# Performance work log

Measured on AMD Instinct MI355X. Metric: run time of the kernel, lower is better.

The kernel has to match this reference:

```python
import jax, jax.numpy as jnp
import numpy as np
import math

SAMPLE_RATIO = 0.25
K = 5
EPS = 1e-6

def _cells(loc_orig, H, W):
    # map normalized [-1,1] coords to nearest grid cell index, as in tcformer token2map/map2token
    loc = jnp.clip(loc_orig, -1.0, 1.0)
    px = jnp.clip(jnp.round(0.5 * (loc[..., 0] + 1.0) * W - 0.5).astype(jnp.int32), 0, W - 1)
    py = jnp.clip(jnp.round(0.5 * (loc[..., 1] + 1.0) * H - 0.5).astype(jnp.int32), 0, H - 1)
    return py * W + px  # [B, N0]

def token2map(x, loc_orig, idx_agg, H, W):
    B, N, C = x.shape
    N0 = loc_orig.shape[1]
    cell = _cells(loc_orig, H, W)
    seg = (cell + jnp.arange(B)[:, None] * (H * W)).reshape(-1)
    feat = x[jnp.arange(B)[:, None], idx_agg]  # [B, N0, C] token feature per original point
    sums = jax.ops.segment_sum(feat.reshape(-1, C), seg, num_segments=B * H * W)
    cnt = jax.ops.segment_sum(jnp.ones((B * N0,), x.dtype), seg, num_segments=B * H * W)
    x_map = sums / (cnt[:, None] + EPS)  # per-cell mean over points hitting the cell
    return x_map.reshape(B, H, W, C).transpose(0, 3, 1, 2)

def map2token(x_map, N, loc_orig, idx_agg, agg_weight):
    B, C, H, W = x_map.shape
    cell = _cells(loc_orig, H, W)
    val = x_map.reshape(B, C, H * W).transpose(0, 2, 1)  # [B, HW, C]
    vpt = val[jnp.arange(B)[:, None], cell]              # [B, N0, C] map value at each point
    seg = (idx_agg + jnp.arange(B)[:, None] * N).reshape(-1)
    w = agg_weight.reshape(-1)
    wsum = jax.ops.segment_sum(w, seg, num_segments=B * N) + EPS
    ssum = jax.ops.segment_sum(vpt.reshape(-1, C) * w[:, None], seg, num_segments=B * N)
    return (ssum / wsum[:, None]).reshape(B, N, C)  # agg_weight-weighted mean per token

def token_cluster_merge(x, Ns, idx_agg, weight, k):
    B, N, C = x.shape
    # DPC-KNN clustering (index computation; mirrors torch.no_grad block)
    sq = jnp.sum(x * x, -1)
    d2 = jnp.clip(sq[:, :, None] + sq[:, None, :] - 2.0 * jnp.einsum('bnc,bmc->bnm', x, x), 0.0, None)
    dist = jnp.sqrt(d2) / (C ** 0.5)
    dnear = -jax.lax.top_k(-dist, k)[0]                  # k smallest distances (incl. self)
    density = jnp.exp(-jnp.mean(dnear * dnear, -1))
    mask = density[:, None, :] > density[:, :, None]
    dmax = jnp.max(dist.reshape(B, -1), -1)[:, None, None]
    parent_dist = jnp.min(jnp.where(mask, dist, dmax), -1)  # dist to nearest higher-density token
    score = parent_dist * density
    index_down = jax.lax.top_k(score, Ns)[1]             # [B, Ns] cluster centers
    idx_cluster = jnp.argmin(dist[jnp.arange(B)[:, None], index_down], axis=1)  # [B, N]
    idx_cluster = idx_cluster.at[jnp.arange(B)[:, None], index_down].set(jnp.arange(Ns)[None, :])
    # weighted merge of tokens into clusters
    seg = (idx_cluster + jnp.arange(B)[:, None] * Ns).reshape(-1)
    w = weight.reshape(-1)
    allw = jax.ops.segment_sum(w, seg, num_segments=B * Ns) + EPS
    norm_w = (w / allw[seg]).reshape(B, N)
    x_merged = jax.ops.segment_sum((x * norm_w[:, :, None]).reshape(-1, C), seg, num_segments=B * Ns).reshape(B, Ns, C)
    idx_agg_down = idx_cluster[jnp.arange(B)[:, None], idx_agg]      # compose index maps
    weight_t = norm_w[jnp.arange(B)[:, None], idx_agg][..., None]    # [B, N0, 1]
    return x_merged, idx_agg_down, weight_t

def _forward(x, loc_orig, idx_agg, agg_weight, idx_k_loc, H, W, conv_w, conv_b, skip_w, ln_g, ln_b, conf_w, conf_b):
    B, N, C = x.shape
    x_map = token2map(x, loc_orig, idx_agg, H, W)
    x_map = jax.lax.conv_general_dilated(x_map, conv_w, (2, 2), ((1, 1), (1, 1))) + conv_b[None, :, None, None]
    x_tok = map2token(x_map, N, loc_orig, idx_agg, agg_weight) + jnp.einsum('bnc,oc->bno', x, skip_w)
    mu = jnp.mean(x_tok, -1, keepdims=True)
    var = jnp.mean((x_tok - mu) ** 2, -1, keepdims=True)
    x_tok = (x_tok - mu) / jnp.sqrt(var + 1e-5) * ln_g + ln_b
    conf = jnp.einsum('bnc,oc->bno', x_tok, conf_w) + conf_b
    weight = jnp.exp(conf)
    Ns = max(math.ceil(N * SAMPLE_RATIO), 1)
    x_down, idx_agg_down, weight_t = token_cluster_merge(x_tok, Ns, idx_agg, weight, K)
    agg_weight_down = agg_weight * weight_t
    agg_weight_down = agg_weight_down / jnp.max(agg_weight_down, axis=1, keepdims=True)
    # down_block is an injected submodule; treated as identity passthrough here
    return x_down, idx_agg_down, agg_weight_down

def setup_inputs():
    key = jax.random.key(0)
    ks = jax.random.split(key, 8)
    B, N, C, N0, Cout = 8, 256, 256, 16384, 512
    return {
        'x': jax.random.normal(ks[0], (B, N, C), jnp.float32),
        'loc_orig': jax.random.uniform(ks[1], (B, N0, 2), jnp.float32, -1.0, 1.0),
        'idx_agg': jax.random.randint(ks[2], (B, N0), 0, N),
        'agg_weight': jax.random.uniform(ks[3], (B, N0, 1), jnp.float32, 0.1, 1.0),
        'idx_k_loc': jax.random.randint(ks[4], (B, N0, K), 0, N0),
        'H': 64, 'W': 64,
        'conv_w': jax.random.normal(ks[5], (Cout, C, 3, 3), jnp.float32) * 0.02,
        'conv_b': jnp.zeros((Cout,), jnp.float32),
        'skip_w': jax.random.normal(ks[6], (Cout, C), jnp.float32) * 0.02,
        'ln_g': jnp.ones((Cout,), jnp.float32),
        'ln_b': jnp.zeros((Cout,), jnp.float32),
        'conf_w': jax.random.normal(ks[7], (1, Cout), jnp.float32) * 0.02,
        'conf_b': jnp.zeros((1,), jnp.float32),
    }

def reference(x, loc_orig, idx_agg, agg_weight, idx_k_loc, H, W, conv_w, conv_b, skip_w, ln_g, ln_b, conf_w, conf_b):
    return _forward(x, loc_orig, idx_agg, agg_weight, idx_k_loc, H, W, conv_w, conv_b, skip_w, ln_g, ln_b, conf_w, conf_b)
```

## Files before the change

kernel.cpp:

```cpp
#include <hip/hip_runtime.h>
#include <math.h>

typedef unsigned long long ull;
typedef __attribute__((ext_vector_type(8))) short short8v;
typedef __attribute__((ext_vector_type(4))) float float4v;

#define NB   8
#define NTOK 256
#define CIN  256
#define NP   16384
#define NCO  512
#define HW64 4096
#define OHW  1024
#define NS   64
#define EPS  1e-6f
#define KC   2304
#define NKC  72

constexpr size_t OFF_SUMS = 0;
constexpr size_t OFF_CNT  = OFF_SUMS + (size_t)NB*HW64*CIN;
constexpr size_t OFF_AMAT = OFF_CNT  + (size_t)NB*HW64;
constexpr size_t OFF_ALLW = OFF_AMAT + (size_t)NB*NTOK*OHW;
constexpr size_t OFF_DMAX = OFF_ALLW + (size_t)NB*NS;
constexpr size_t OFF_MAXW = OFF_DMAX + NB;
constexpr size_t ZERO_END = OFF_MAXW + NB;
constexpr size_t OFF_WT   = ZERO_END;
constexpr size_t OFF_SKWT = OFF_WT   + (size_t)KC*NCO;
constexpr size_t OFF_Y    = OFF_SKWT + (size_t)CIN*NCO;
constexpr size_t OFF_C2   = OFF_Y    + (size_t)NB*OHW*NCO;
constexpr size_t OFF_WSUM = OFF_C2   + (size_t)NB*NTOK*NCO;
constexpr size_t OFF_XSKIP= OFF_WSUM + (size_t)NB*NTOK;
constexpr size_t OFF_XTOK = OFF_XSKIP+ (size_t)NB*NTOK*NCO;
constexpr size_t OFF_XPK  = OFF_XTOK + (size_t)NB*NTOK*NCO;
constexpr size_t OFF_WEXP = OFF_XPK  + (size_t)NB*NTOK*NCO;
constexpr size_t OFF_SQ   = OFF_WEXP + (size_t)NB*NTOK;
constexpr size_t OFF_DIST = OFF_SQ   + (size_t)NB*NTOK;
constexpr size_t OFF_DENS = OFF_DIST + (size_t)NB*NTOK*NTOK;
constexpr size_t OFF_SCORE= OFF_DENS + (size_t)NB*NTOK;
constexpr size_t OFF_IND  = OFF_SCORE+ (size_t)NB*NTOK;
constexpr size_t OFF_IDXCL= OFF_IND  + (size_t)NB*NS;
constexpr size_t OFF_NORMW= OFF_IDXCL+ (size_t)NB*NTOK;
constexpr size_t OFF_AWBUF= OFF_NORMW+ (size_t)NB*NTOK;
constexpr size_t OFF_XTPK = OFF_AWBUF+ (size_t)NB*NP;
constexpr size_t OFF_XTOKPK= OFF_Y;

__device__ __forceinline__ unsigned pack_hl(float x) {
    unsigned u = __float_as_uint(x);
    unsigned t = u + 0x7fffu + ((u >> 16) & 1u);
    unsigned hibits = t & 0xffff0000u;
    float lo = x - __uint_as_float(hibits);
    unsigned ul = __float_as_uint(lo);
    unsigned lt = ul + 0x7fffu + ((ul >> 16) & 1u);
    return hibits | (lt >> 16);
}
__device__ __forceinline__ unsigned f2bf(float f) {
    unsigned u = __float_as_uint(f);
    return (u + 0x7fffu + ((u >> 16) & 1u)) >> 16;
}
__device__ __forceinline__ unsigned hp2(unsigned w0, unsigned w1) {
    return __builtin_amdgcn_perm(w1, w0, 0x07060302u);
}
__device__ __forceinline__ unsigned lp2(unsigned w0, unsigned w1) {
    return __builtin_amdgcn_perm(w1, w0, 0x05040100u);
}

__global__ void hist(const float* __restrict__ loc, const int* __restrict__ idxagg,
                     const float* __restrict__ aggw,
                     int* __restrict__ cntmat, float* __restrict__ cnt,
                     float* __restrict__ amat) {
    int bp = blockIdx.x*256 + threadIdx.x;
    int b  = bp >> 14;
    float lx = loc[2*bp+0], ly = loc[2*bp+1];
    lx = fminf(fmaxf(lx, -1.f), 1.f);
    ly = fminf(fmaxf(ly, -1.f), 1.f);
    int px = (int)rintf((lx + 1.f)*32.f - 0.5f); px = min(max(px,0),63);
    int py = (int)rintf((ly + 1.f)*32.f - 0.5f); py = min(max(py,0),63);
    int cell = py*64 + px;
    int tok = idxagg[bp];
    atomicAdd(&cntmat[((size_t)(b*HW64 + cell))*NTOK + tok], 1);
    atomicAdd(&cnt[b*HW64 + cell], 1.0f);
    int qx = (int)rintf((lx + 1.f)*16.f - 0.5f); qx = min(max(qx,0),31);
    int qy = (int)rintf((ly + 1.f)*16.f - 0.5f); qy = min(max(qy,0),31);
    atomicAdd(&amat[((size_t)(b*NTOK + tok))*OHW + qy*32 + qx], aggw[bp]);
}

__global__ void xpack_both(const float* __restrict__ x, unsigned* __restrict__ xtpk,
                           unsigned* __restrict__ xpk) {
    int id = blockIdx.x*256 + threadIdx.x;
    int tok = id & 255, cin = (id >> 8) & 255, b = id >> 16;
    unsigned pk = pack_hl(x[((size_t)(b*NTOK + tok))*CIN + cin]);
    xtpk[id] = pk;
    xpk[((size_t)(b*NTOK + tok))*CIN + cin] = pk;
}

__global__ void wtrans(const float* __restrict__ convw, uint4* __restrict__ wtf) {
    int tid = blockIdx.x*256 + threadIdx.x;
    int lane = tid & 63;
    int r1 = tid >> 6;
    int h = r1 & 1;
    int r2 = r1 >> 1;
    int f = r2 & 3;
    int r3 = r2 >> 2;
    int kc = r3 % NKC, mt = r3 / NKC;
    int cout = mt*64 + f*16 + (lane & 15);
    int kb = kc*32 + (lane >> 4)*8;
    unsigned s[8];
    #pragma unroll
    for (int j = 0; j < 8; ++j) {
        int k = kb + j;
        int grp = k >> 8, cin = k & 255;
        unsigned w = pack_hl(convw[(size_t)cout*KC + cin*9 + grp]);
        s[j] = h ? (w & 0xffffu) : (w >> 16);
    }
    uint4 o;
    o.x = s[0] | (s[1]<<16); o.y = s[2] | (s[3]<<16);
    o.z = s[4] | (s[5]<<16); o.w = s[6] | (s[7]<<16);
    wtf[tid] = o;
}

__global__ void pack4(const float4* __restrict__ src, uint4* __restrict__ dst) {
    size_t i = (size_t)blockIdx.x*256 + threadIdx.x;
    float4 v = src[i];
    uint4 o;
    o.x = pack_hl(v.x); o.y = pack_hl(v.y); o.z = pack_hl(v.z); o.w = pack_hl(v.w);
    dst[i] = o;
}

__launch_bounds__(512)
__global__ void map_gemm(const int* __restrict__ A, const unsigned* __restrict__ B,
                         const float* __restrict__ cnt, unsigned* __restrict__ xmapu) {
    __shared__ __align__(16) unsigned short Ah[4096];
    __shared__ __align__(16) unsigned short Bh[8192], Bl[8192];
    int z = blockIdx.z, m0 = blockIdx.y*128;
    const int* Ab = A + ((size_t)z*HW64 + m0)*NTOK;
    const unsigned* Bb = B + (size_t)z*CIN*NTOK;
    int t = threadIdx.x, lane = t & 63;
    int w = t >> 6;
    int wm = w >> 2, wn = w & 3;
    int l15 = lane & 15, l4 = lane >> 4;
    int rowA = t & 127, kgA = t >> 7;
    int rowB = t & 255, kgB0 = (t >> 8)*2;
    const int* arow = Ab + (size_t)rowA*NTOK + kgA*8;
    const unsigned* brow = Bb + (size_t)rowB*NTOK + kgB0*8;
    int wbA = (rowA>>4)*512 + kgA*128 + (rowA&15)*8;
    int wbB = (rowB>>4)*512 + kgB0*128 + (rowB&15)*8;

    float4v acc[4][4] = {};
    int4 ia0, ia1;
    uint4 rb[2][2];
    auto loadA = [&](int kc) {
        const int* p = arow + kc*32;
        ia0 = *(const int4*)p; ia1 = *(const int4*)(p + 4);
    };
    auto loadB = [&](int kc) {
        #pragma unroll
        for (int s = 0; s < 2; ++s) {
            const unsigned* p = brow + kc*32 + s*8;
            rb[s][0] = *(const uint4*)p; rb[s][1] = *(const uint4*)(p + 4);
        }
    };
    loadA(0); loadB(0);

    for (int kc = 0; kc < 8; ++kc) {
        __syncthreads();
        uint4 h, l;
        h.x = f2bf((float)ia0.x) | (f2bf((float)ia0.y) << 16);
        h.y = f2bf((float)ia0.z) | (f2bf((float)ia0.w) << 16);
        h.z = f2bf((float)ia1.x) | (f2bf((float)ia1.y) << 16);
        h.w = f2bf((float)ia1.z) | (f2bf((float)ia1.w) << 16);
        *(uint4*)&Ah[wbA] = h;
        #pragma unroll
        for (int s = 0; s < 2; ++s) {
            uint4 u0 = rb[s][0], u1 = rb[s][1];
            h.x=hp2(u0.x,u0.y); h.y=hp2(u0.z,u0.w); h.z=hp2(u1.x,u1.y); h.w=hp2(u1.z,u1.w);
            l.x=lp2(u0.x,u0.y); l.y=lp2(u0.z,u0.w); l.z=lp2(u1.x,u1.y); l.w=lp2(u1.z,u1.w);
            *(uint4*)&Bh[wbB + s*128] = h; *(uint4*)&Bl[wbB + s*128] = l;
        }
        __syncthreads();
        if (kc < 7) { loadA(kc+1); loadB(kc+1); }

        short8v bh[4], bl[4];
        #pragma unroll
        for (int q = 0; q < 4; ++q) {
            int off = (wn*4 + q)*512 + l4*128 + l15*8;
            bh[q] = *(const short8v*)&Bh[off];
            bl[q] = *(const short8v*)&Bl[off];
        }
        #pragma unroll
        for (int p = 0; p < 4; ++p) {
            int off = (wm*4 + p)*512 + l4*128 + l15*8;
            short8v ah = *(const short8v*)&Ah[off];
            #pragma unroll
            for (int q = 0; q < 4; ++q) {
                acc[p][q] = __builtin_amdgcn_mfma_f32_16x16x32_bf16(ah, bh[q], acc[p][q], 0, 0, 0);
                acc[p][q] = __builtin_amdgcn_mfma_f32_16x16x32_bf16(ah, bl[q], acc[p][q], 0, 0, 0);
            }
        }
    }

    const float* cntb = cnt + (size_t)z*HW64;
    #pragma unroll
    for (int p = 0; p < 4; ++p) {
        int mb = m0 + wm*64 + p*16 + l4*4;
        #pragma unroll
        for (int q = 0; q < 4; ++q) {
            int n = wn*64 + q*16 + l15;
            #pragma unroll
            for (int r = 0; r < 4; ++r) {
                float v = acc[p][q][r] / (cntb[mb + r] + EPS);
                xmapu[((size_t)z*HW64 + mb + r)*CIN + n] = pack_hl(v);
            }
        }
    }
}

__launch_bounds__(256)
__global__ void conv_gemm(const unsigned* __restrict__ xmap, const uint4* __restrict__ wtf,
                          const float* __restrict__ convb, unsigned* __restrict__ ytp) {
    __shared__ __align__(16) unsigned short Ahi[2][4096], Alo[2][4096];
    int bid = blockIdx.x;
    int mt = bid & 7;
    int xt = bid >> 3;
    int n0 = xt * 128;
    int m0 = mt * 64;
    int t = threadIdx.x;
    int lane = t & 63, wid = t >> 6;
    int wm = wid >> 1, wn = wid & 1;
    int l15 = lane & 15, l4 = lane >> 4;

    int rowL = t & 127, kg = t >> 7;
    int posG = n0 + rowL;
    int bb = posG >> 10, rem = posG & 1023;
    int oy = rem >> 5, ox = rem & 31;

    int wbA0 = (rowL>>4)*512 + kg*128 + (rowL&15)*8;
    int wbA1 = wbA0 + 256;

    float4v acc[4][2] = {};
    uint4 a00,a01,a10,a11;

    auto loadA = [&](int kc) {
        int grp = kc >> 3;
        int ky = grp/3, kx = grp - 3*ky;
        int iy = 2*oy - 1 + ky, ix = 2*ox - 1 + kx;
        if ((unsigned)iy < 64u && (unsigned)ix < 64u) {
            const unsigned* ap = xmap + ((((size_t)bb*64 + iy)*64 + ix)*256 + (kc&7)*32 + kg*8);
            a00 = *(const uint4*)ap;       a01 = *(const uint4*)(ap + 4);
            a10 = *(const uint4*)(ap + 16); a11 = *(const uint4*)(ap + 20);
        } else {
            a00 = make_uint4(0,0,0,0); a01 = a00; a10 = a00; a11 = a00;
        }
    };
    auto repackA = [&](int buf) {
        uint4 h, l;
        h.x=hp2(a00.x,a00.y); h.y=hp2(a00.z,a00.w); h.z=hp2(a01.x,a01.y); h.w=hp2(a01.z,a01.w);
        l.x=lp2(a00.x,a00.y); l.y=lp2(a00.z,a00.w); l.z=lp2(a01.x,a01.y); l.w=lp2(a01.z,a01.w);
        *(uint4*)&Ahi[buf][wbA0] = h; *(uint4*)&Alo[buf][wbA0] = l;
        h.x=hp2(a10.x,a10.y); h.y=hp2(a10.z,a10.w); h.z=hp2(a11.x,a11.y); h.w=hp2(a11.z,a11.w);
        l.x=lp2(a10.x,a10.y); l.y=lp2(a10.z,a10.w); l.z=lp2(a11.x,a11.y); l.w=lp2(a11.z,a11.w);
        *(uint4*)&Ahi[buf][wbA1] = h; *(uint4*)&Alo[buf][wbA1] = l;
    };
    const uint4* wbase = wtf + ((size_t)(((mt*NKC)*4 + wn*2)*2))*64 + lane;

    short8v bhc[2], blc[2], bhn[2], bln[2];
    #pragma unroll
    for (int q = 0; q < 2; ++q) {
        bhc[q] = *(const short8v*)(wbase + q*128);
        blc[q] = *(const short8v*)(wbase + q*128 + 64);
    }
    loadA(0);
    repackA(0);
    __syncthreads();
    int cur = 0;

    for (int kc = 0; kc < NKC; ++kc) {
        bool nl = (kc + 1 < NKC);
        if (nl) {
            loadA(kc+1);
            const uint4* wb = wbase + (size_t)(kc+1)*512;
            #pragma unroll
            for (int q = 0; q < 2; ++q) {
                bhn[q] = *(const short8v*)(wb + q*128);
                bln[q] = *(const short8v*)(wb + q*128 + 64);
            }
        }
        #pragma unroll
        for (int p = 0; p < 4; ++p) {
            int off = (wm*4 + p)*512 + l4*128 + l15*8;
            short8v ah = *(const short8v*)&Ahi[cur][off];
            short8v al = *(const short8v*)&Alo[cur][off];
            #pragma unroll
            for (int q = 0; q < 2; ++q) {
                acc[p][q] = __builtin_amdgcn_mfma_f32_16x16x32_bf16(ah, bhc[q], acc[p][q], 0, 0, 0);
                acc[p][q] = __builtin_amdgcn_mfma_f32_16x16x32_bf16(ah, blc[q], acc[p][q], 0, 0, 0);
                acc[p][q] = __builtin_amdgcn_mfma_f32_16x16x32_bf16(al, bhc[q], acc[p][q], 0, 0, 0);
            }
        }
        if (nl) {
            repackA(cur ^ 1);
            #pragma unroll
            for (int q = 0; q < 2; ++q) { bhc[q] = bhn[q]; blc[q] = bln[q]; }
        }
        __syncthreads();
        cur ^= 1;
    }

    int bbk = n0 >> 10;
    int pos0 = (n0 & 1023) + wm*64;
    #pragma unroll
    for (int p = 0; p < 4; ++p) {
        int posb = pos0 + p*16 + l4*4;
        #pragma unroll
        for (int q = 0; q < 2; ++q) {
            int col = m0 + wn*32 + q*16 + l15;
            float bv = convb[col];
            uint4 o;
            o.x = pack_hl(acc[p][q][0] + bv);
            o.y = pack_hl(acc[p][q][1] + bv);
            o.z = pack_hl(acc[p][q][2] + bv);
            o.w = pack_hl(acc[p][q][3] + bv);
            *(uint4*)&ytp[((size_t)(bbk*NCO + col))*OHW + posb] = o;
        }
    }
}

template<int MODE, int TM, int TN, int AF>
__launch_bounds__(256)
__global__ void gemm_pk(const void* __restrict__ Av, const unsigned* __restrict__ B,
                        float* __restrict__ C, int K, int N,
                        long sA, long sB, long sC,
                        const float* __restrict__ aux, unsigned* __restrict__ dmaxU) {
    constexpr int NA = TM/64, NBs = TN/64;
    constexpr int WSM = TM/64;
    constexpr int WSN = 4/WSM;
    constexpr int TWM = TM/WSM, TWN = TN/WSN;
    constexpr int P = TWM/16, Q = TWN/16;
    __shared__ __align__(16) unsigned short Ahi[TM*32], Alo[TM*32];
    __shared__ __align__(16) unsigned short Bhi[TN*32], Blo[TN*32];
    int z = blockIdx.z;
    const unsigned* Ab = (const unsigned*)Av + (size_t)z*sA;
    const unsigned* Bb = B + (size_t)z*sB;
    float* Cb = C + (size_t)z*sC;
    int n0 = blockIdx.x*TN, m0 = blockIdx.y*TM;
    int t = threadIdx.x;
    int lane = t & 63, wid = t >> 6;
    int wm = (WSM==2) ? (wid >> 1) : 0;
    int wn = (WSM==2) ? (wid & 1)  : wid;
    int l15 = lane & 15, l4 = lane >> 4;

    int rowA = t & (TM-1), kgA = t / TM;
    int rowB = t & (TN-1), kgB = t / TN;
    const unsigned* arow = Ab + (size_t)(m0 + rowA)*K + kgA*8;
    const unsigned* brw  = Bb + (size_t)(n0 + rowB)*K + kgB*8;
    int wbA = (rowA>>4)*512 + kgA*128 + (rowA&15)*8;
    int wbB = (rowB>>4)*512 + kgB*128 + (rowB&15)*8;

    float4v acc[P][Q] = {};
    uint4 ra[NA][2], rb[NBs][2];
    auto loadA = [&](int kc) {
        #pragma unroll
        for (int s = 0; s < NA; ++s) {
            const unsigned* p = arow + (size_t)kc*32 + s*16;
            ra[s][0] = *(const uint4*)p; ra[s][1] = *(const uint4*)(p + 4);
        }
    };
    auto loadB = [&](int kc) {
        #pragma unroll
        for (int s = 0; s < NBs; ++s) {
            const unsigned* p = brw + (size_t)kc*32 + s*16;
            rb[s][0] = *(const uint4*)p; rb[s][1] = *(const uint4*)(p + 4);
        }
    };
    loadA(0); loadB(0);
    int nkc = K >> 5;

    for (int kc = 0; kc < nkc; ++kc) {
        __syncthreads();
        uint4 h, l;
        #pragma unroll
        for (int s = 0; s < NA; ++s) {
            uint4 u0 = ra[s][0], u1 = ra[s][1];
            if (AF == 0) {
                h.x=hp2(u0.x,u0.y); h.y=hp2(u0.z,u0.w); h.z=hp2(u1.x,u1.y); h.w=hp2(u1.z,u1.w);
                l.x=lp2(u0.x,u0.y); l.y=lp2(u0.z,u0.w); l.z=lp2(u1.x,u1.y); l.w=lp2(u1.z,u1.w);
            } else {
                unsigned pk0 = pack_hl(__uint_as_float(u0.x)), pk1 = pack_hl(__uint_as_float(u0.y));
                unsigned pk2 = pack_hl(__uint_as_float(u0.z)), pk3 = pack_hl(__uint_as_float(u0.w));
                unsigned pk4 = pack_hl(__uint_as_float(u1.x)), pk5 = pack_hl(__uint_as_float(u1.y));
                unsigned pk6 = pack_hl(__uint_as_float(u1.z)), pk7 = pack_hl(__uint_as_float(u1.w));
                h.x = (pk0>>16) | (pk1 & 0xffff0000u); h.y = (pk2>>16) | (pk3 & 0xffff0000u);
                h.z = (pk4>>16) | (pk5 & 0xffff0000u); h.w = (pk6>>16) | (pk7 & 0xffff0000u);
                l.x = (pk0&0xffffu) | (pk1<<16); l.y = (pk2&0xffffu) | (pk3<<16);
                l.z = (pk4&0xffffu) | (pk5<<16); l.w = (pk6&0xffffu) | (pk7<<16);
            }
            *(uint4*)&Ahi[wbA + s*256] = h; *(uint4*)&Alo[wbA + s*256] = l;
        }
        #pragma unroll
        for (int s = 0; s < NBs; ++s) {
            uint4 u0 = rb[s][0], u1 = rb[s][1];
            h.x=hp2(u0.x,u0.y); h.y=hp2(u0.z,u0.w); h.z=hp2(u1.x,u1.y); h.w=hp2(u1.z,u1.w);
            l.x=lp2(u0.x,u0.y); l.y=lp2(u0.z,u0.w); l.z=lp2(u1.x,u1.y); l.w=lp2(u1.z,u1.w);
            *(uint4*)&Bhi[wbB + s*256] = h; *(uint4*)&Blo[wbB + s*256] = l;
        }
        __syncthreads();
        if (kc + 1 < nkc) { loadA(kc+1); loadB(kc+1); }

        short8v bh[Q], bl[Q];
        #pragma unroll
        for (int q = 0; q < Q; ++q) {
            int off = (wn*Q + q)*512 + l4*128 + l15*8;
            bh[q] = *(const short8v*)&Bhi[off];
            bl[q] = *(const short8v*)&Blo[off];
        }
        #pragma unroll
        for (int p = 0; p < P; ++p) {
            int off = (wm*P + p)*512 + l4*128 + l15*8;
            short8v ah = *(const short8v*)&Ahi[off];
            short8v al = *(const short8v*)&Alo[off];
            #pragma unroll
            for (int q = 0; q < Q; ++q) {
                acc[p][q] = __builtin_amdgcn_mfma_f32_16x16x32_bf16(ah, bh[q], acc[p][q], 0, 0, 0);
                acc[p][q] = __builtin_amdgcn_mfma_f32_16x16x32_bf16(ah, bl[q], acc[p][q], 0, 0, 0);
                acc[p][q] = __builtin_amdgcn_mfma_f32_16x16x32_bf16(al, bh[q], acc[p][q], 0, 0, 0);
            }
        }
    }

    if (MODE == 0) {
        #pragma unroll
        for (int p = 0; p < P; ++p) {
            int mb = m0 + wm*TWM + p*16 + l4*4;
            #pragma unroll
            for (int q = 0; q < Q; ++q) {
                int n = n0 + wn*TWN + q*16 + l15;
                #pragma unroll
                for (int r = 0; r < 4; ++r)
                    Cb[(size_t)(mb + r)*N + n] = acc[p][q][r];
            }
        }
    } else {
        const float inv = 1.0f / sqrtf(512.0f);
        const float* sqb = aux + (size_t)z*NTOK;
        float tmax = 0.f;
        #pragma unroll
        for (int p = 0; p < P; ++p) {
            int mb = m0 + wm*TWM + p*16 + l4*4;
            #pragma unroll
            for (int q = 0; q < Q; ++q) {
                int n = n0 + wn*TWN + q*16 + l15;
                float sn = sqb[n];
                #pragma unroll
                for (int r = 0; r < 4; ++r) {
                    float d2 = sqb[mb + r] + sn - 2.0f*acc[p][q][r];
                    float d = sqrtf(fmaxf(d2, 0.0f)) * inv;
                    Cb[(size_t)(mb + r)*N + n] = d;
                    tmax = fmaxf(tmax, d);
                }
            }
        }
        __shared__ float redm[4];
        #pragma unroll
        for (int off = 32; off; off >>= 1) tmax = fmaxf(tmax, __shfl_xor(tmax, off, 64));
        if (lane == 0) redm[wid] = tmax;
        __syncthreads();
        if (t == 0) {
            float m = fmaxf(fmaxf(redm[0], redm[1]), fmaxf(redm[2], redm[3]));
            atomicMax(dmaxU + z, __float_as_uint(m));
        }
    }
}

__global__ void wsum_rows(const float* __restrict__ amat, float* __restrict__ wsum) {
    int row = blockIdx.x*4 + (threadIdx.x >> 6);
    int lane = threadIdx.x & 63;
    const float* ar = amat + (size_t)row*OHW;
    float s = 0.f;
    #pragma unroll
    for (int r = 0; r < 16; ++r) s += ar[lane + 64*r];
    #pragma unroll
    for (int off = 32; off; off >>= 1) s += __shfl_xor(s, off, 64);
    if (lane == 0) wsum[row] = s;
}

__device__ __forceinline__ float block_sum256(float v, float* red) {
    #pragma unroll
    for (int off = 32; off; off >>= 1) v += __shfl_xor(v, off, 64);
    __syncthreads();
    if ((threadIdx.x & 63) == 0) red[threadIdx.x >> 6] = v;
    __syncthreads();
    return red[0] + red[1] + red[2] + red[3];
}

__global__ void ln_conf(const float* __restrict__ C2, const float* __restrict__ wsum,
                        const float* __restrict__ xskip, const float* __restrict__ g,
                        const float* __restrict__ be, const float* __restrict__ confw,
                        const float* __restrict__ confb, float* __restrict__ xtok,
                        unsigned* __restrict__ xtokpk,
                        float* __restrict__ wexp, float* __restrict__ sqv) {
    __shared__ float red[4];
    int row = blockIdx.x, t = threadIdx.x;
    float ws = wsum[row] + EPS;
    size_t base = (size_t)row*NCO;
    float v0 = C2[base + t]       / ws + xskip[base + t];
    float v1 = C2[base + t + 256] / ws + xskip[base + t + 256];
    float mu  = block_sum256(v0 + v1, red) / 512.0f;
    float d0 = v0 - mu, d1 = v1 - mu;
    float var = block_sum256(d0*d0 + d1*d1, red) / 512.0f;
    float sv = sqrtf(var + 1e-5f);
    float x0 = d0/sv * g[t]       + be[t];
    float x1 = d1/sv * g[t + 256] + be[t + 256];
    xtok[base + t] = x0;
    xtok[base + t + 256] = x1;
    xtokpk[base + t] = pack_hl(x0);
    xtokpk[base + t + 256] = pack_hl(x1);
    float cs = block_sum256(x0*confw[t] + x1*confw[t + 256], red);
    float qs = block_sum256(x0*x0 + x1*x1, red);
    if (t == 0) {
        wexp[row] = expf(cs + confb[0]);
        sqv[row]  = qs;
    }
}

__global__ void knn_dens(const float* __restrict__ dist, float* __restrict__ dens) {
    int row = blockIdx.x*4 + (threadIdx.x >> 6);
    int lane = threadIdx.x & 63;
    const float* dr = dist + (size_t)row*NTOK;
    float v0 = dr[lane], v1 = dr[lane+64], v2 = dr[lane+128], v3 = dr[lane+192];
    float acc = 0.f;
    #pragma unroll
    for (int it = 0; it < 5; ++it) {
        float lm = fminf(fminf(v0, v1), fminf(v2, v3));
        float gm = lm;
        #pragma unroll
        for (int off = 32; off; off >>= 1) gm = fminf(gm, __shfl_xor(gm, off, 64));
        acc += gm*gm;
        ull ball = __ballot(lm == gm);
        int first = __ffsll(ball) - 1;
        if (lane == first) {
            if      (v0 == gm) v0 = 1e30f;
            else if (v1 == gm) v1 = 1e30f;
            else if (v2 == gm) v2 = 1e30f;
            else               v3 = 1e30f;
        }
    }
    if (lane == 0) dens[row] = expf(-(acc/5.0f));
}

__global__ void parent_score(const float* __restrict__ dist, const float* __restrict__ dens,
                             const unsigned* __restrict__ dmaxU, float* __restrict__ score) {
    int row = blockIdx.x*4 + (threadIdx.x >> 6);
    int lane = threadIdx.x & 63;
    int b = row >> 8;
    float di = dens[row];
    float dm = __uint_as_float(dmaxU[b]);
    const float* dr = dist + (size_t)row*NTOK;
    const float* db = dens + (size_t)b*NTOK;
    float pd = dm;
    #pragma unroll
    for (int r = 0; r < 4; ++r) {
        int j = lane + 64*r;
        pd = fminf(pd, (db[j] > di) ? dr[j] : dm);
    }
    #pragma unroll
    for (int off = 32; off; off >>= 1) pd = fminf(pd, __shfl_xor(pd, off, 64));
    if (lane == 0) score[row] = pd * di;
}

__global__ void topk64(const float* __restrict__ score, int* __restrict__ ind) {
    int b = blockIdx.x, lane = threadIdx.x;
    const float* sb = score + b*NTOK;
    ull k0, k1, k2, k3;
    {
        unsigned i0 = lane, i1 = lane+64, i2 = lane+128, i3 = lane+192;
        k0 = ((ull)(__float_as_uint(sb[i0]) + 1u) << 32) | (unsigned)(4095 - i0);
        k1 = ((ull)(__float_as_uint(sb[i1]) + 1u) << 32) | (unsigned)(4095 - i1);
        k2 = ((ull)(__float_as_uint(sb[i2]) + 1u) << 32) | (unsigned)(4095 - i2);
        k3 = ((ull)(__float_as_uint(sb[i3]) + 1u) << 32) | (unsigned)(4095 - i3);
    }
    for (int it = 0; it < 64; ++it) {
        ull lm = k0;
        if (k1 > lm) lm = k1;
        if (k2 > lm) lm = k2;
        if (k3 > lm) lm = k3;
        ull gm = lm;
        #pragma unroll
        for (int off = 32; off; off >>= 1) {
            ull o = __shfl_xor(gm, off, 64);
            if (o > gm) gm = o;
        }
        if (lane == 0) ind[b*NS + it] = 4095 - (int)(gm & 0xffffffffull);
        if      (k0 == gm) k0 = 0;
        else if (k1 == gm) k1 = 0;
        else if (k2 == gm) k2 = 0;
        else if (k3 == gm) k3 = 0;
    }
}

__global__ void assign_k(const float* __restrict__ dist, const int* __restrict__ ind,
                         int* __restrict__ idxcl) {
    int row = blockIdx.x*4 + (threadIdx.x >> 6);
    int lane = threadIdx.x & 63;
    int b = row >> 8, i = row & 255;
    int center = ind[b*NS + lane];
    float d = dist[((size_t)(b*NTOK + center))*NTOK + i];
    ull key = ((ull)__float_as_uint(d) << 32) | (unsigned)lane;
    #pragma unroll
    for (int off = 32; off; off >>= 1) {
        ull o = __shfl_xor(key, off, 64);
        if (o < key) key = o;
    }
    if (lane == 0) idxcl[row] = (int)(key & 0xffffffffull);
}

__global__ void center_set(const int* __restrict__ ind, int* __restrict__ idxcl) {
    int id = threadIdx.x;
    int b = id >> 6, s = id & 63;
    idxcl[b*NTOK + ind[id]] = s;
}

__global__ void allw_acc(const int* __restrict__ idxcl, const float* __restrict__ wexp,
                         float* __restrict__ allw) {
    int b = blockIdx.x, i = threadIdx.x;
    atomicAdd(&allw[b*NS + idxcl[b*NTOK + i]], wexp[b*NTOK + i]);
}

__global__ void normw_k(const int* __restrict__ idxcl, const float* __restrict__ wexp,
                        const float* __restrict__ allw, float* __restrict__ normw) {
    int b = blockIdx.x, i = threadIdx.x;
    normw[b*NTOK + i] = wexp[b*NTOK + i] / (allw[b*NS + idxcl[b*NTOK + i]] + EPS);
}

__global__ void merge_k(const float* __restrict__ xtok, const int* __restrict__ idxcl,
                        const float* __restrict__ normw, float* __restrict__ xout) {
    int row = blockIdx.x, t = threadIdx.x;
    int b = row >> 8;
    int cl = idxcl[row];
    float nw = normw[row];
    float* o = xout + ((size_t)(b*NS + cl))*NCO;
    const float* xr = xtok + (size_t)row*NCO;
    atomicAdd(&o[t],       xr[t]       * nw);
    atomicAdd(&o[t + 256], xr[t + 256] * nw);
}

__global__ void out_idx_aw(const int* __restrict__ idxagg, const float* __restrict__ aggw,
                           const int* __restrict__ idxcl, const float* __restrict__ normw,
                           float* __restrict__ dout, float* __restrict__ awbuf,
                           unsigned* __restrict__ maxw) {
    __shared__ float red[4];
    int bp = blockIdx.x*256 + threadIdx.x;
    int b = bp >> 14;
    int tok = idxagg[bp];
    int cl = idxcl[b*NTOK + tok];
    dout[(size_t)NB*NS*NCO + bp] = (float)cl;
    float aw = aggw[bp] * normw[b*NTOK + tok];
    awbuf[bp] = aw;
    float m = aw;
    #pragma unroll
    for (int off = 32; off; off >>= 1) m = fmaxf(m, __shfl_xor(m, off, 64));
    if ((threadIdx.x & 63) == 0) red[threadIdx.x >> 6] = m;
    __syncthreads();
    if (threadIdx.x == 0) {
        float mm = fmaxf(fmaxf(red[0], red[1]), fmaxf(red[2], red[3]));
        atomicMax(&maxw[b], __float_as_uint(mm));
    }
}

__global__ void aw_final(const float* __restrict__ awbuf, const float* __restrict__ maxw,
                         float* __restrict__ dout) {
    int bp = blockIdx.x*256 + threadIdx.x;
    int b = bp >> 14;
    dout[(size_t)NB*NS*NCO + (size_t)NB*NP + bp] = awbuf[bp] / maxw[b];
}

extern "C" void kernel_launch(void* const* d_in, const int* in_sizes, int n_in,
                              void* d_out, int out_size, void* d_ws, size_t ws_size,
                              hipStream_t stream) {
    const float* x      = (const float*)d_in[0];
    const float* loc    = (const float*)d_in[1];
    const int*   idxagg = (const int*)  d_in[2];
    const float* aggw   = (const float*)d_in[3];
    const float* convw  = (const float*)d_in[7];
    const float* convb  = (const float*)d_in[8];
    const float* skipw  = (const float*)d_in[9];
    const float* lng    = (const float*)d_in[10];
    const float* lnb    = (const float*)d_in[11];
    const float* confw  = (const float*)d_in[12];
    const float* confb  = (const float*)d_in[13];

    float* ws = (float*)d_ws;
    float* dout = (float*)d_out;

    (void)hipMemsetAsync(ws, 0, ZERO_END*sizeof(float), stream);
    (void)hipMemsetAsync(dout, 0, (size_t)NB*NS*NCO*sizeof(float), stream);

    hist<<<dim3(NB*NP/256), 256, 0, stream>>>(loc, idxagg, aggw,
                                              (int*)(ws + OFF_SUMS), ws + OFF_CNT, ws + OFF_AMAT);
    xpack_both<<<dim3(NB*CIN*NTOK/256), 256, 0, stream>>>(x, (unsigned*)(ws + OFF_XTPK),
                                                          (unsigned*)(ws + OFF_XPK));
    wtrans<<<dim3(1152), 256, 0, stream>>>(convw, (uint4*)(ws + OFF_WT));
    pack4<<<dim3(CIN*NCO/1024), 256, 0, stream>>>((const float4*)skipw, (uint4*)(ws + OFF_SKWT));

    map_gemm<<<dim3(1, 32, 8), 512, 0, stream>>>((const int*)(ws + OFF_SUMS),
                                                 (const unsigned*)(ws + OFF_XTPK),
                                                 ws + OFF_CNT,
                                                 (unsigned*)(ws + OFF_SUMS));

    conv_gemm<<<dim3(512), 256, 0, stream>>>((const unsigned*)(ws + OFF_SUMS),
                                             (const uint4*)(ws + OFF_WT), convb,
                                             (unsigned*)(ws + OFF_Y));

    wsum_rows<<<dim3(NB*NTOK/4), 256, 0, stream>>>(ws + OFF_AMAT, ws + OFF_WSUM);
    gemm_pk<0,64,64,1><<<dim3(8, 4, 8), 256, 0, stream>>>((const void*)(ws + OFF_AMAT),
                                                  (const unsigned*)(ws + OFF_Y),
                                                  ws + OFF_C2, OHW, NCO,
                                                  (long)NTOK*OHW, (long)NCO*OHW, (long)NTOK*NCO,
                                                  nullptr, nullptr);
    gemm_pk<0,64,64,0><<<dim3(8, 32, 1), 256, 0, stream>>>((const void*)(ws + OFF_XPK),
                                                   (const unsigned*)(ws + OFF_SKWT),
                                                   ws + OFF_XSKIP, CIN, NCO, 0, 0, 0,
                                                   nullptr, nullptr);

    ln_conf<<<dim3(NB*NTOK), 256, 0, stream>>>(ws + OFF_C2, ws + OFF_WSUM, ws + OFF_XSKIP,
                                               lng, lnb, confw, confb,
                                               ws + OFF_XTOK, (unsigned*)(ws + OFF_XTOKPK),
                                               ws + OFF_WEXP, ws + OFF_SQ);

    gemm_pk<1,64,64,0><<<dim3(4, 4, 8), 256, 0, stream>>>((const void*)(ws + OFF_XTOKPK),
                                                  (const unsigned*)(ws + OFF_XTOKPK),
                                                  ws + OFF_DIST, NCO, NTOK,
                                                  (long)NTOK*NCO, (long)NTOK*NCO, (long)NTOK*NTOK,
                                                  ws + OFF_SQ, (unsigned*)(ws + OFF_DMAX));

    knn_dens<<<dim3(NB*NTOK/4), 256, 0, stream>>>(ws + OFF_DIST, ws + OFF_DENS);
    parent_score<<<dim3(NB*NTOK/4), 256, 0, stream>>>(ws + OFF_DIST, ws + OFF_DENS,
                                                      (const unsigned*)(ws + OFF_DMAX), ws + OFF_SCORE);
    topk64<<<dim3(NB), 64, 0, stream>>>(ws + OFF_SCORE, (int*)(ws + OFF_IND));
    assign_k<<<dim3(NB*NTOK/4), 256, 0, stream>>>(ws + OFF_DIST, (const int*)(ws + OFF_IND),
                                                  (int*)(ws + OFF_IDXCL));
    center_set<<<dim3(1), 512, 0, stream>>>((const int*)(ws + OFF_IND), (int*)(ws + OFF_IDXCL));
    allw_acc<<<dim3(NB), 256, 0, stream>>>((const int*)(ws + OFF_IDXCL), ws + OFF_WEXP, ws + OFF_ALLW);
    normw_k<<<dim3(NB), 256, 0, stream>>>((const int*)(ws + OFF_IDXCL), ws + OFF_WEXP,
                                          ws + OFF_ALLW, ws + OFF_NORMW);
    merge_k<<<dim3(NB*NTOK), 256, 0, stream>>>(ws + OFF_XTOK, (const int*)(ws + OFF_IDXCL),
                                               ws + OFF_NORMW, dout);
    out_idx_aw<<<dim3(NB*NP/256), 256, 0, stream>>>(idxagg, aggw, (const int*)(ws + OFF_IDXCL),
                                                    ws + OFF_NORMW, dout, ws + OFF_AWBUF,
                                                    (unsigned*)(ws + OFF_MAXW));
    aw_final<<<dim3(NB*NP/256), 256, 0, stream>>>(ws + OFF_AWBUF, (const float*)(ws + OFF_MAXW), dout);
}
```

Baseline: 306.4 us.

## Fuse clustering tail kernels into one per-batch kernel; deepen conv A-prefetch

The seven small clustering kernels (knn density, parent score, top-k, assignment, center set, weight accumulation, normalization) become one kernel with one block per batch, holding intermediates in shared memory. This removes several launches and global round-trips. The price is that the work now runs on only 8 blocks of 256 threads. The conv GEMM loop is also unrolled by two with two register sets for A, so global loads are issued two stages ahead, and the grid moves to a 2D layout that changes block ordering.

```diff
diff --git a/kernel.cpp b/kernel.cpp
--- a/kernel.cpp
+++ b/kernel.cpp
@@ -218,10 +218,8 @@
 __global__ void conv_gemm(const unsigned* __restrict__ xmap, const uint4* __restrict__ wtf,
                           const float* __restrict__ convb, unsigned* __restrict__ ytp) {
     __shared__ __align__(16) unsigned short Ahi[2][4096], Alo[2][4096];
-    int bid = blockIdx.x;
-    int mt = bid & 7;
-    int xt = bid >> 3;
-    int n0 = xt * 128;
+    int n0 = blockIdx.x * 128;
+    int mt = blockIdx.y;
     int m0 = mt * 64;
     int t = threadIdx.x;
     int lane = t & 63, wid = t >> 6;
@@ -237,27 +235,46 @@
     int wbA1 = wbA0 + 256;
 
     float4v acc[4][2] = {};
-    uint4 a00,a01,a10,a11;
-
-    auto loadA = [&](int kc) {
+    uint4 aA0,aA1,aA2,aA3;
+    uint4 aB0,aB1,aB2,aB3;
+
+    auto addrA = [&](int kc, int* ok) -> const unsigned* {
         int grp = kc >> 3;
         int ky = grp/3, kx = grp - 3*ky;
         int iy = 2*oy - 1 + ky, ix = 2*ox - 1 + kx;
-        if ((unsigned)iy < 64u && (unsigned)ix < 64u) {
-            const unsigned* ap = xmap + ((((size_t)bb*64 + iy)*64 + ix)*256 + (kc&7)*32 + kg*8);
-            a00 = *(const uint4*)ap;       a01 = *(const uint4*)(ap + 4);
-            a10 = *(const uint4*)(ap + 16); a11 = *(const uint4*)(ap + 20);
-        } else {
-            a00 = make_uint4(0,0,0,0); a01 = a00; a10 = a00; a11 = a00;
-        }
-    };
-    auto repackA = [&](int buf) {
+        *ok = ((unsigned)iy < 64u) && ((unsigned)ix < 64u);
+        return xmap + ((((size_t)bb*64 + iy)*64 + ix)*256 + (kc&7)*32 + kg*8);
+    };
+    auto loadA_A = [&](int kc) {
+        int ok; const unsigned* ap = addrA(kc, &ok);
+        if (ok) {
+            aA0 = *(const uint4*)ap;       aA1 = *(const uint4*)(ap + 4);
+            aA2 = *(const uint4*)(ap + 16); aA3 = *(const uint4*)(ap + 20);
+        } else { aA0 = make_uint4(0,0,0,0); aA1 = aA0; aA2 = aA0; aA3 = aA0; }
+    };
+    auto loadA_B = [&](int kc) {
+        int ok; const unsigned* ap = addrA(kc, &ok);
+        if (ok) {
+            aB0 = *(const uint4*)ap;       aB1 = *(const uint4*)(ap + 4);
+            aB2 = *(const uint4*)(ap + 16); aB3 = *(const uint4*)(ap + 20);
+        } else { aB0 = make_uint4(0,0,0,0); aB1 = aB0; aB2 = aB0; aB3 = aB0; }
+    };
+    auto repack_A = [&](int buf) {
         uint4 h, l;
-        h.x=hp2(a00.x,a00.y); h.y=hp2(a00.z,a00.w); h.z=hp2(a01.x,a01.y); h.w=hp2(a01.z,a01.w);
-        l.x=lp2(a00.x,a00.y); l.y=lp2(a00.z,a00.w); l.z=lp2(a01.x,a01.y); l.w=lp2(a01.z,a01.w);
+        h.x=hp2(aA0.x,aA0.y); h.y=hp2(aA0.z,aA0.w); h.z=hp2(aA1.x,aA1.y); h.w=hp2(aA1.z,aA1.w);
+        l.x=lp2(aA0.x,aA0.y); l.y=lp2(aA0.z,aA0.w); l.z=lp2(aA1.x,aA1.y); l.w=lp2(aA1.z,aA1.w);
         *(uint4*)&Ahi[buf][wbA0] = h; *(uint4*)&Alo[buf][wbA0] = l;
-        h.x=hp2(a10.x,a10.y); h.y=hp2(a10.z,a10.w); h.z=hp2(a11.x,a11.y); h.w=hp2(a11.z,a11.w);
-        l.x=lp2(a10.x,a10.y); l.y=lp2(a10.z,a10.w); l.z=lp2(a11.x,a11.y); l.w=lp2(a11.z,a11.w);
+        h.x=hp2(aA2.x,aA2.y); h.y=hp2(aA2.z,aA2.w); h.z=hp2(aA3.x,aA3.y); h.w=hp2(aA3.z,aA3.w);
+        l.x=lp2(aA2.x,aA2.y); l.y=lp2(aA2.z,aA2.w); l.z=lp2(aA3.x,aA3.y); l.w=lp2(aA3.z,aA3.w);
+        *(uint4*)&Ahi[buf][wbA1] = h; *(uint4*)&Alo[buf][wbA1] = l;
+    };
+    auto repack_B = [&](int buf) {
+        uint4 h, l;
+        h.x=hp2(aB0.x,aB0.y); h.y=hp2(aB0.z,aB0.w); h.z=hp2(aB1.x,aB1.y); h.w=hp2(aB1.z,aB1.w);
+        l.x=lp2(aB0.x,aB0.y); l.y=lp2(aB0.z,aB0.w); l.z=lp2(aB1.x,aB1.y); l.w=lp2(aB1.z,aB1.w);
+        *(uint4*)&Ahi[buf][wbA0] = h; *(uint4*)&Alo[buf][wbA0] = l;
+        h.x=hp2(aB2.x,aB2.y); h.y=hp2(aB2.z,aB2.w); h.z=hp2(aB3.x,aB3.y); h.w=hp2(aB3.z,aB3.w);
+        l.x=lp2(aB2.x,aB2.y); l.y=lp2(aB2.z,aB2.w); l.z=lp2(aB3.x,aB3.y); l.w=lp2(aB3.z,aB3.w);
         *(uint4*)&Ahi[buf][wbA1] = h; *(uint4*)&Alo[buf][wbA1] = l;
     };
     const uint4* wbase = wtf + ((size_t)(((mt*NKC)*4 + wn*2)*2))*64 + lane;
@@ -268,15 +285,29 @@
         bhc[q] = *(const short8v*)(wbase + q*128);
         blc[q] = *(const short8v*)(wbase + q*128 + 64);
     }
-    loadA(0);
-    repackA(0);
+    loadA_B(0);
+    repack_B(0);
+    loadA_A(1);
     __syncthreads();
     int cur = 0;
 
-    for (int kc = 0; kc < NKC; ++kc) {
-        bool nl = (kc + 1 < NKC);
-        if (nl) {
-            loadA(kc+1);
+    #define CONV_MFMA_BLOCK                                                            \
+        _Pragma("unroll")                                                              \
+        for (int p = 0; p < 4; ++p) {                                                  \
+            int off = (wm*4 + p)*512 + l4*128 + l15*8;                                 \
+            short8v ah = *(const short8v*)&Ahi[cur][off];                              \
+            short8v al = *(const short8v*)&Alo[cur][off];                              \
+            _Pragma("unroll")                                                          \
+            for (int q = 0; q < 2; ++q) {                                              \
+                acc[p][q] = __builtin_amdgcn_mfma_f32_16x16x32_bf16(ah, bhc[q], acc[p][q], 0, 0, 0); \
+                acc[p][q] = __builtin_amdgcn_mfma_f32_16x16x32_bf16(ah, blc[q], acc[p][q], 0, 0, 0); \
+                acc[p][q] = __builtin_amdgcn_mfma_f32_16x16x32_bf16(al, bhc[q], acc[p][q], 0, 0, 0); \
+            }                                                                          \
+        }
+
+    for (int kc = 0; kc < NKC; kc += 2) {
+        if (kc + 2 < NKC) loadA_B(kc + 2);
+        {
             const uint4* wb = wbase + (size_t)(kc+1)*512;
             #pragma unroll
             for (int q = 0; q < 2; ++q) {
@@ -284,26 +315,33 @@
                 bln[q] = *(const short8v*)(wb + q*128 + 64);
             }
         }
-        #pragma unroll
-        for (int p = 0; p < 4; ++p) {
-            int off = (wm*4 + p)*512 + l4*128 + l15*8;
-            short8v ah = *(const short8v*)&Ahi[cur][off];
-            short8v al = *(const short8v*)&Alo[cur][off];
-            #pragma unroll
-            for (int q = 0; q < 2; ++q) {
-                acc[p][q] = __builtin_amdgcn_mfma_f32_16x16x32_bf16(ah, bhc[q], acc[p][q], 0, 0, 0);
-                acc[p][q] = __builtin_amdgcn_mfma_f32_16x16x32_bf16(ah, blc[q], acc[p][q], 0, 0, 0);
-                acc[p][q] = __builtin_amdgcn_mfma_f32_16x16x32_bf16(al, bhc[q], acc[p][q], 0, 0, 0);
-            }
-        }
-        if (nl) {
-            repackA(cur ^ 1);
-            #pragma unroll
-            for (int q = 0; q < 2; ++q) { bhc[q] = bhn[q]; blc[q] = bln[q]; }
-        }
+        CONV_MFMA_BLOCK
+        repack_A(cur ^ 1);
+        #pragma unroll
+        for (int q = 0; q < 2; ++q) { bhc[q] = bhn[q]; blc[q] = bln[q]; }
         __syncthreads();
         cur ^= 1;
-    }
+
+        int k1 = kc + 1;
+        if (k1 + 2 < NKC) loadA_A(k1 + 2);
+        if (k1 + 1 < NKC) {
+            const uint4* wb = wbase + (size_t)(k1+1)*512;
+            #pragma unroll
+            for (int q = 0; q < 2; ++q) {
+                bhn[q] = *(const short8v*)(wb + q*128);
+                bln[q] = *(const short8v*)(wb + q*128 + 64);
+            }
+        }
+        CONV_MFMA_BLOCK
+        if (k1 + 1 < NKC) {
+            repack_B(cur ^ 1);
+            #pragma unroll
+            for (int q = 0; q < 2; ++q) { bhc[q] = bhn[q]; blc[q] = bln[q]; }
+        }
+        __syncthreads();
+        cur ^= 1;
+    }
+    #undef CONV_MFMA_BLOCK
 
     int bbk = n0 >> 10;
     int pos0 = (n0 & 1023) + wm*64;
@@ -521,113 +559,106 @@
     }
 }
 
-__global__ void knn_dens(const float* __restrict__ dist, float* __restrict__ dens) {
-    int row = blockIdx.x*4 + (threadIdx.x >> 6);
-    int lane = threadIdx.x & 63;
-    const float* dr = dist + (size_t)row*NTOK;
-    float v0 = dr[lane], v1 = dr[lane+64], v2 = dr[lane+128], v3 = dr[lane+192];
-    float acc = 0.f;
-    #pragma unroll
-    for (int it = 0; it < 5; ++it) {
-        float lm = fminf(fminf(v0, v1), fminf(v2, v3));
-        float gm = lm;
-        #pragma unroll
-        for (int off = 32; off; off >>= 1) gm = fminf(gm, __shfl_xor(gm, off, 64));
-        acc += gm*gm;
-        ull ball = __ballot(lm == gm);
-        int first = __ffsll(ball) - 1;
-        if (lane == first) {
-            if      (v0 == gm) v0 = 1e30f;
-            else if (v1 == gm) v1 = 1e30f;
-            else if (v2 == gm) v2 = 1e30f;
-            else               v3 = 1e30f;
-        }
-    }
-    if (lane == 0) dens[row] = expf(-(acc/5.0f));
-}
-
-__global__ void parent_score(const float* __restrict__ dist, const float* __restrict__ dens,
-                             const unsigned* __restrict__ dmaxU, float* __restrict__ score) {
-    int row = blockIdx.x*4 + (threadIdx.x >> 6);
-    int lane = threadIdx.x & 63;
-    int b = row >> 8;
-    float di = dens[row];
+__launch_bounds__(256)
+__global__ void cluster_tail(const float* __restrict__ dist, const unsigned* __restrict__ dmaxU,
+                             const float* __restrict__ wexp,
+                             int* __restrict__ idxcl_g, float* __restrict__ normw_g) {
+    __shared__ float densL[NTOK], scoreL[NTOK], allwL[NS];
+    __shared__ int indL[NS], idxclL[NTOK];
+    int b = blockIdx.x, t = threadIdx.x;
+    int lane = t & 63, w = t >> 6;
+    const float* db = dist + (size_t)b*NTOK*NTOK;
+    const float* we = wexp + (size_t)b*NTOK;
+
+    for (int r = w; r < NTOK; r += 4) {
+        const float* dr = db + (size_t)r*NTOK;
+        float v0 = dr[lane], v1 = dr[lane+64], v2 = dr[lane+128], v3 = dr[lane+192];
+        float acc = 0.f;
+        #pragma unroll
+        for (int it = 0; it < 5; ++it) {
+            float lm = fminf(fminf(v0, v1), fminf(v2, v3));
+            float gm = lm;
+            #pragma unroll
+            for (int off = 32; off; off >>= 1) gm = fminf(gm, __shfl_xor(gm, off, 64));
+            acc += gm*gm;
+            ull ball = __ballot(lm == gm);
+            int first = __ffsll(ball) - 1;
+            if (lane == first) {
+                if      (v0 == gm) v0 = 1e30f;
+                else if (v1 == gm) v1 = 1e30f;
+                else if (v2 == gm) v2 = 1e30f;
+                else               v3 = 1e30f;
+            }
+        }
+        if (lane == 0) densL[r] = expf(-(acc/5.0f));
+    }
+    __syncthreads();
+
     float dm = __uint_as_float(dmaxU[b]);
-    const float* dr = dist + (size_t)row*NTOK;
-    const float* db = dens + (size_t)b*NTOK;
-    float pd = dm;
-    #pragma unroll
-    for (int r = 0; r < 4; ++r) {
-        int j = lane + 64*r;
-        pd = fminf(pd, (db[j] > di) ? dr[j] : dm);
-    }
-    #pragma unroll
-    for (int off = 32; off; off >>= 1) pd = fminf(pd, __shfl_xor(pd, off, 64));
-    if (lane == 0) score[row] = pd * di;
-}
-
-__global__ void topk64(const float* __restrict__ score, int* __restrict__ ind) {
-    int b = blockIdx.x, lane = threadIdx.x;
-    const float* sb = score + b*NTOK;
-    ull k0, k1, k2, k3;
-    {
+    for (int r = w; r < NTOK; r += 4) {
+        const float* dr = db + (size_t)r*NTOK;
+        float di = densL[r];
+        float pd = dm;
+        #pragma unroll
+        for (int c = 0; c < 4; ++c) {
+            int j = lane + 64*c;
+            pd = fminf(pd, (densL[j] > di) ? dr[j] : dm);
+        }
+        #pragma unroll
+        for (int off = 32; off; off >>= 1) pd = fminf(pd, __shfl_xor(pd, off, 64));
+        if (lane == 0) scoreL[r] = pd * di;
+    }
+    __syncthreads();
+
+    if (w == 0) {
+        ull k0, k1, k2, k3;
         unsigned i0 = lane, i1 = lane+64, i2 = lane+128, i3 = lane+192;
-        k0 = ((ull)(__float_as_uint(sb[i0]) + 1u) << 32) | (unsigned)(4095 - i0);
-        k1 = ((ull)(__float_as_uint(sb[i1]) + 1u) << 32) | (unsigned)(4095 - i1);
-        k2 = ((ull)(__float_as_uint(sb[i2]) + 1u) << 32) | (unsigned)(4095 - i2);
-        k3 = ((ull)(__float_as_uint(sb[i3]) + 1u) << 32) | (unsigned)(4095 - i3);
-    }
-    for (int it = 0; it < 64; ++it) {
-        ull lm = k0;
-        if (k1 > lm) lm = k1;
-        if (k2 > lm) lm = k2;
-        if (k3 > lm) lm = k3;
-        ull gm = lm;
+        k0 = ((ull)(__float_as_uint(scoreL[i0]) + 1u) << 32) | (unsigned)(4095 - i0);
+        k1 = ((ull)(__float_as_uint(scoreL[i1]) + 1u) << 32) | (unsigned)(4095 - i1);
+        k2 = ((ull)(__float_as_uint(scoreL[i2]) + 1u) << 32) | (unsigned)(4095 - i2);
+        k3 = ((ull)(__float_as_uint(scoreL[i3]) + 1u) << 32) | (unsigned)(4095 - i3);
+        for (int it = 0; it < NS; ++it) {
+            ull lm = k0;
+            if (k1 > lm) lm = k1;
+            if (k2 > lm) lm = k2;
+            if (k3 > lm) lm = k3;
+            ull gm = lm;
+            #pragma unroll
+            for (int off = 32; off; off >>= 1) {
+                ull o = __shfl_xor(gm, off, 64);
+                if (o > gm) gm = o;
+            }
+            if (lane == 0) indL[it] = 4095 - (int)(gm & 0xffffffffull);
+            if      (k0 == gm) k0 = 0;
+            else if (k1 == gm) k1 = 0;
+            else if (k2 == gm) k2 = 0;
+            else if (k3 == gm) k3 = 0;
+        }
+    }
+    __syncthreads();
+
+    int myc = indL[lane];
+    for (int r = w; r < NTOK; r += 4) {
+        float d = db[(size_t)myc*NTOK + r];
+        ull key = ((ull)__float_as_uint(d) << 32) | (unsigned)lane;
         #pragma unroll
         for (int off = 32; off; off >>= 1) {
-            ull o = __shfl_xor(gm, off, 64);
-            if (o > gm) gm = o;
-        }
-        if (lane == 0) ind[b*NS + it] = 4095 - (int)(gm & 0xffffffffull);
-        if      (k0 == gm) k0 = 0;
-        else if (k1 == gm) k1 = 0;
-        else if (k2 == gm) k2 = 0;
-        else if (k3 == gm) k3 = 0;
-    }
-}
-
-__global__ void assign_k(const float* __restrict__ dist, const int* __restrict__ ind,
-                         int* __restrict__ idxcl) {
-    int row = blockIdx.x*4 + (threadIdx.x >> 6);
-    int lane = threadIdx.x & 63;
-    int b = row >> 8, i = row & 255;
-    int center = ind[b*NS + lane];
-    float d = dist[((size_t)(b*NTOK + center))*NTOK + i];
-    ull key = ((ull)__float_as_uint(d) << 32) | (unsigned)lane;
-    #pragma unroll
-    for (int off = 32; off; off >>= 1) {
-        ull o = __shfl_xor(key, off, 64);
-        if (o < key) key = o;
-    }
-    if (lane == 0) idxcl[row] = (int)(key & 0xffffffffull);
-}
-
-__global__ void center_set(const int* __restrict__ ind, int* __restrict__ idxcl) {
-    int id = threadIdx.x;
-    int b = id >> 6, s = id & 63;
-    idxcl[b*NTOK + ind[id]] = s;
-}
-
-__global__ void allw_acc(const int* __restrict__ idxcl, const float* __restrict__ wexp,
-                         float* __restrict__ allw) {
-    int b = blockIdx.x, i = threadIdx.x;
-    atomicAdd(&allw[b*NS + idxcl[b*NTOK + i]], wexp[b*NTOK + i]);
-}
-
-__global__ void normw_k(const int* __restrict__ idxcl, const float* __restrict__ wexp,
-                        const float* __restrict__ allw, float* __restrict__ normw) {
-    int b = blockIdx.x, i = threadIdx.x;
-    normw[b*NTOK + i] = wexp[b*NTOK + i] / (allw[b*NS + idxcl[b*NTOK + i]] + EPS);
+            ull o = __shfl_xor(key, off, 64);
+            if (o < key) key = o;
+        }
+        if (lane == 0) idxclL[r] = (int)(key & 0xffffffffull);
+    }
+    __syncthreads();
+
+    if (t < NS) idxclL[indL[t]] = t;
+    if (t < NS) allwL[t] = 0.f;
+    __syncthreads();
+
+    atomicAdd(&allwL[idxclL[t]], we[t]);
+    __syncthreads();
+
+    normw_g[(size_t)b*NTOK + t] = we[t] / (allwL[idxclL[t]] + EPS);
+    idxcl_g[(size_t)b*NTOK + t] = idxclL[t];
 }
 
 __global__ void merge_k(const float* __restrict__ xtok, const int* __restrict__ idxcl,
@@ -705,9 +736,9 @@
                                                  ws + OFF_CNT,
                                                  (unsigned*)(ws + OFF_SUMS));
 
-    conv_gemm<<<dim3(512), 256, 0, stream>>>((const unsigned*)(ws + OFF_SUMS),
-                                             (const uint4*)(ws + OFF_WT), convb,
-                                             (unsigned*)(ws + OFF_Y));
+    conv_gemm<<<dim3(64, 8), 256, 0, stream>>>((const unsigned*)(ws + OFF_SUMS),
+                                               (const uint4*)(ws + OFF_WT), convb,
+                                               (unsigned*)(ws + OFF_Y));
 
     wsum_rows<<<dim3(NB*NTOK/4), 256, 0, stream>>>(ws + OFF_AMAT, ws + OFF_WSUM);
     gemm_pk<0,64,64,1><<<dim3(8, 4, 8), 256, 0, stream>>>((const void*)(ws + OFF_AMAT),
@@ -731,16 +762,11 @@
                                                   (long)NTOK*NCO, (long)NTOK*NCO, (long)NTOK*NTOK,
                                                   ws + OFF_SQ, (unsigned*)(ws + OFF_DMAX));
 
-    knn_dens<<<dim3(NB*NTOK/4), 256, 0, stream>>>(ws + OFF_DIST, ws + OFF_DENS);
-    parent_score<<<dim3(NB*NTOK/4), 256, 0, stream>>>(ws + OFF_DIST, ws + OFF_DENS,
-                                                      (const unsigned*)(ws + OFF_DMAX), ws + OFF_SCORE);
-    topk64<<<dim3(NB), 64, 0, stream>>>(ws + OFF_SCORE, (int*)(ws + OFF_IND));
-    assign_k<<<dim3(NB*NTOK/4), 256, 0, stream>>>(ws + OFF_DIST, (const int*)(ws + OFF_IND),
-                                                  (int*)(ws + OFF_IDXCL));
-    center_set<<<dim3(1), 512, 0, stream>>>((const int*)(ws + OFF_IND), (int*)(ws + OFF_IDXCL));
-    allw_acc<<<dim3(NB), 256, 0, stream>>>((const int*)(ws + OFF_IDXCL), ws + OFF_WEXP, ws + OFF_ALLW);
-    normw_k<<<dim3(NB), 256, 0, stream>>>((const int*)(ws + OFF_IDXCL), ws + OFF_WEXP,
-                                          ws + OFF_ALLW, ws + OFF_NORMW);
+    cluster_tail<<<dim3(NB), 256, 0, stream>>>(ws + OFF_DIST,
+                                               (const unsigned*)(ws + OFF_DMAX),
+                                               ws + OFF_WEXP,
+                                               (int*)(ws + OFF_IDXCL), ws + OFF_NORMW);
+
     merge_k<<<dim3(NB*NTOK), 256, 0, stream>>>(ws + OFF_XTOK, (const int*)(ws + OFF_IDXCL),
                                                ws + OFF_NORMW, dout);
     out_idx_aw<<<dim3(NB*NP/256), 256, 0, stream>>>(idxagg, aggw, (const int*)(ws + OFF_IDXCL),
```

New measurement: 444.9 us. 1.45x slower.
